# Optimization experiments

Measured on AMD Instinct MI355X. Metric: run time of the kernel, lower is better.

Reference implementation:

```python
import jax, jax.numpy as jnp
import numpy as np

N_NODES = 50000
N_EDGES = 800000
NUM_GRAPHS = 512


def gcn_conv(x, edge_index, W, b, num_nodes):
    # PyG GCNConv: h = D^{-1/2} (A + I) D^{-1/2} (x @ W) + b
    h = x @ W
    src, dst = edge_index[0], edge_index[1]
    loop = jnp.arange(num_nodes)
    src = jnp.concatenate([src, loop])
    dst = jnp.concatenate([dst, loop])
    deg = jax.ops.segment_sum(jnp.ones_like(dst, dtype=h.dtype), dst,
                              num_segments=num_nodes)
    dinv = jnp.where(deg > 0, jax.lax.rsqrt(deg), 0.0)
    norm = dinv[src] * dinv[dst]                      # [E+N]
    msg = h[src] * norm[:, None]                      # gather + scale
    out = jax.ops.segment_sum(msg, dst, num_segments=num_nodes)  # scatter-add
    return out + b


def global_mean_pool(x, batch, num_graphs):
    sums = jax.ops.segment_sum(x, batch, num_segments=num_graphs)
    cnts = jax.ops.segment_sum(jnp.ones((x.shape[0],), x.dtype), batch,
                               num_segments=num_graphs)
    return sums / jnp.maximum(cnts, 1.0)[:, None]


def setup_inputs() -> dict:
    key = jax.random.key(0)
    ks = jax.random.split(key, 8)
    x = jax.random.normal(ks[0], (N_NODES, 128), dtype=jnp.float32)
    edge_index = jax.random.randint(ks[1], (2, N_EDGES), 0, N_NODES, dtype=jnp.int64)
    batch = jnp.sort(jax.random.randint(ks[2], (N_NODES,), 0, NUM_GRAPHS, dtype=jnp.int64))
    W1 = jax.random.normal(ks[3], (128, 128), dtype=jnp.float32) * (1.0 / np.sqrt(128))
    b1 = jnp.zeros((128,), jnp.float32)
    W2 = jax.random.normal(ks[4], (128, 64), dtype=jnp.float32) * (1.0 / np.sqrt(128))
    b2 = jnp.zeros((64,), jnp.float32)
    Wl = jax.random.normal(ks[5], (64, 64), dtype=jnp.float32) * (1.0 / np.sqrt(64))
    bl = jnp.zeros((64,), jnp.float32)
    return {"x": x, "edge_index": edge_index, "batch": batch,
            "W1": W1, "b1": b1, "W2": W2, "b2": b2, "Wl": Wl, "bl": bl}


def reference(x, edge_index, batch, W1, b1, W2, b2, Wl, bl):
    num_nodes = x.shape[0]
    h = gcn_conv(x, edge_index, W1, b1, num_nodes)
    h = jax.nn.relu(h)
    h = gcn_conv(h, edge_index, W2, b2, num_nodes)
    g = global_mean_pool(h, batch, NUM_GRAPHS)
    # dropout p=0.5 is identity in eval mode
    return g @ Wl + bl
```

## Files before the change

### kernel.cpp

```cpp
#include <hip/hip_runtime.h>
#include <hip/hip_fp16.h>
#include <math.h>


#define FEAT1 128
#define FEAT2 64
#define BCAP 8192

using half8 = __attribute__((ext_vector_type(8))) _Float16;
using half4 = __attribute__((ext_vector_type(4))) _Float16;
using f32x4 = __attribute__((ext_vector_type(4))) float;


__global__ __launch_bounds__(256) void bin_scatter(const int* __restrict__ esrc,
                                                   const int* __restrict__ edst,
                                                   int ne, int nb,
                                                   int* __restrict__ bucket_cursor,
                                                   int* __restrict__ ebin) {
    __shared__ int lcnt[256];
    __shared__ int lcur[256];
    const int tid = threadIdx.x;
    const int e0 = blockIdx.x * 8192;
    lcnt[tid] = 0;
    __syncthreads();
    #pragma unroll 4
    for (int k = 0; k < 32; k++) {
        int e = e0 + k * 256 + tid;
        if (e < ne) atomicAdd(&lcnt[edst[e] >> 8], 1);
    }
    __syncthreads();
    if (tid < nb && lcnt[tid] > 0)
        lcur[tid] = atomicAdd(&bucket_cursor[tid], lcnt[tid]);
    __syncthreads();
    #pragma unroll 4
    for (int k = 0; k < 32; k++) {
        int e = e0 + k * 256 + tid;
        if (e < ne) {
            int d = edst[e];
            int b = d >> 8;
            int p = atomicAdd(&lcur[b], 1);
            if (p < BCAP)
                ebin[b * BCAP + p] = esrc[e] | ((d & 255) << 18);
        }
    }
}

__global__ __launch_bounds__(256) void bucket_csr(const int* __restrict__ ebin,
                                                  const int* __restrict__ bucket_cursor,
                                                  int n_nodes,
                                                  int* __restrict__ csr,
                                                  int2* __restrict__ nodeinfo,
                                                  float* __restrict__ dinv) {
    __shared__ int lcnt[256];
    __shared__ int lscan[256];
    __shared__ int lcur[256];
    const int b = blockIdx.x;
    const int tid = threadIdx.x;
    const int ebeg = b * BCAP;
    int cnt_b = bucket_cursor[b];
    if (cnt_b > BCAP) cnt_b = BCAP;
    const int eend = ebeg + cnt_b;
    lcnt[tid] = 0;
    __syncthreads();
    for (int e = ebeg + tid; e < eend; e += 256)
        atomicAdd(&lcnt[(ebin[e] >> 18) & 255], 1);
    __syncthreads();
    int v = lcnt[tid];
    lscan[tid] = v;
    __syncthreads();
    for (int off = 1; off < 256; off <<= 1) {
        int u = (tid >= off) ? lscan[tid - off] : 0;
        __syncthreads();
        lscan[tid] += u;
        __syncthreads();
    }
    const int start = ebeg + (lscan[tid] - v);
    const int node = (b << 8) + tid;
    if (node < n_nodes) {
        nodeinfo[node] = make_int2(start, v);
        dinv[node] = (float)(1.0 / sqrt((double)(v + 1)));
    }
    lcur[tid] = start;
    __syncthreads();
    for (int e = ebeg + tid; e < eend; e += 256) {
        int pk = ebin[e];
        int p = atomicAdd(&lcur[(pk >> 18) & 255], 1);
        csr[p] = pk & 0x3FFFF;
    }
}

template <int FOUT, bool A_F16>
__global__ __launch_bounds__(256) void gemm_mfma(const void* __restrict__ Aptr,
                                                 const float* __restrict__ W,
                                                 const float* __restrict__ dinv,
                                                 _Float16* __restrict__ out, int n) {
    __shared__ _Float16 As[128 * 136];
    __shared__ _Float16 Ws[64 * 136];
    const int tid = threadIdx.x;
    const int wv = tid >> 6;
    const int lane = tid & 63;
    constexpr int NCT = FOUT / 64;
    const int row0 = blockIdx.x * 128;

    {
        const int r = tid >> 1;
        const int c0 = (tid & 1) * 64;
        const int grow = row0 + r;
        if constexpr (A_F16) {
            const _Float16* A = (const _Float16*)Aptr + (size_t)grow * 128 + c0;
            #pragma unroll
            for (int j = 0; j < 8; j++) {
                half8 v = {};
                if (grow < n) v = *(const half8*)(A + j * 8);
                *(half8*)(&As[r * 136 + c0 + j * 8]) = v;
            }
        } else {
            const float* A = (const float*)Aptr + (size_t)grow * 128 + c0;
            #pragma unroll
            for (int j = 0; j < 16; j++) {
                float4 v = {0.f, 0.f, 0.f, 0.f};
                if (grow < n) v = *(const float4*)(A + j * 4);
                half4 hv = {(_Float16)v.x, (_Float16)v.y, (_Float16)v.z, (_Float16)v.w};
                *(half4*)(&As[r * 136 + c0 + j * 4]) = hv;
            }
        }
    }

    for (int ct = 0; ct < NCT; ct++) {
        const int col0 = ct * 64;
        __syncthreads();
        {
            const int k = tid >> 1;
            const int cb = (tid & 1) * 32;
            #pragma unroll
            for (int j = 0; j < 8; j++) {
                int c = cb + j * 4;
                float4 v = *(const float4*)(W + (size_t)k * FOUT + col0 + c);
                Ws[(c + 0) * 136 + k] = (_Float16)v.x;
                Ws[(c + 1) * 136 + k] = (_Float16)v.y;
                Ws[(c + 2) * 136 + k] = (_Float16)v.z;
                Ws[(c + 3) * 136 + k] = (_Float16)v.w;
            }
        }
        __syncthreads();

        f32x4 acc[2][4] = {};
        const int mrow = wv * 32 + (lane & 15);
        const int kb = (lane >> 4) * 8;
        #pragma unroll
        for (int ks = 0; ks < 4; ks++) {
            const int kk = ks * 32 + kb;
            half8 a0 = *(const half8*)(&As[mrow * 136 + kk]);
            half8 a1 = *(const half8*)(&As[(mrow + 16) * 136 + kk]);
            #pragma unroll
            for (int nj = 0; nj < 4; nj++) {
                half8 b = *(const half8*)(&Ws[(nj * 16 + (lane & 15)) * 136 + kk]);
                acc[0][nj] = __builtin_amdgcn_mfma_f32_16x16x32_f16(a0, b, acc[0][nj], 0, 0, 0);
                acc[1][nj] = __builtin_amdgcn_mfma_f32_16x16x32_f16(a1, b, acc[1][nj], 0, 0, 0);
            }
        }

        #pragma unroll
        for (int mi = 0; mi < 2; mi++) {
            const int gr0 = row0 + wv * 32 + mi * 16 + (lane >> 4) * 4;
            #pragma unroll
            for (int r = 0; r < 4; r++) {
                const int grow = gr0 + r;
                if (grow < n) {
                    const float s = dinv[grow];
                    #pragma unroll
                    for (int nj = 0; nj < 4; nj++) {
                        out[(size_t)grow * FOUT + col0 + nj * 16 + (lane & 15)] =
                            (_Float16)(acc[mi][nj][r] * s);
                    }
                }
            }
        }
    }
}

template <int F, bool RELU, bool OUT16>
__global__ __launch_bounds__(256) void aggregate_h(const __half* __restrict__ t,
                                                   const float* __restrict__ dinv,
                                                   const int2* __restrict__ nodeinfo,
                                                   const int* __restrict__ csr_src,
                                                   const float* __restrict__ bias,
                                                   void* __restrict__ outp, int n) {
    const int wv = threadIdx.x >> 6;
    const int lane = threadIdx.x & 63;
    const int i = blockIdx.x * 4 + wv;
    if (i >= n) return;
    const float di = dinv[i];
    const int2 ni = nodeinfo[i];
    const int e0 = ni.x, e1 = ni.x + ni.y;

    if constexpr (F == 128) {
        float2 a0, a1 = {0.f, 0.f}, a2 = {0.f, 0.f}, a3 = {0.f, 0.f};
        a0 = __half22float2(((const __half2*)(t + (size_t)i * F))[lane]);
        int e = e0;
        for (; e + 8 <= e1; e += 8) {
            int s0 = csr_src[e + 0], s1 = csr_src[e + 1], s2 = csr_src[e + 2], s3 = csr_src[e + 3];
            int s4 = csr_src[e + 4], s5 = csr_src[e + 5], s6 = csr_src[e + 6], s7 = csr_src[e + 7];
            float2 v0 = __half22float2(((const __half2*)(t + (size_t)s0 * F))[lane]);
            float2 v1 = __half22float2(((const __half2*)(t + (size_t)s1 * F))[lane]);
            float2 v2 = __half22float2(((const __half2*)(t + (size_t)s2 * F))[lane]);
            float2 v3 = __half22float2(((const __half2*)(t + (size_t)s3 * F))[lane]);
            float2 v4 = __half22float2(((const __half2*)(t + (size_t)s4 * F))[lane]);
            float2 v5 = __half22float2(((const __half2*)(t + (size_t)s5 * F))[lane]);
            float2 v6 = __half22float2(((const __half2*)(t + (size_t)s6 * F))[lane]);
            float2 v7 = __half22float2(((const __half2*)(t + (size_t)s7 * F))[lane]);
            a0.x += v0.x + v4.x; a0.y += v0.y + v4.y;
            a1.x += v1.x + v5.x; a1.y += v1.y + v5.y;
            a2.x += v2.x + v6.x; a2.y += v2.y + v6.y;
            a3.x += v3.x + v7.x; a3.y += v3.y + v7.y;
        }
        for (; e + 4 <= e1; e += 4) {
            int s0 = csr_src[e + 0], s1 = csr_src[e + 1], s2 = csr_src[e + 2], s3 = csr_src[e + 3];
            float2 v0 = __half22float2(((const __half2*)(t + (size_t)s0 * F))[lane]);
            float2 v1 = __half22float2(((const __half2*)(t + (size_t)s1 * F))[lane]);
            float2 v2 = __half22float2(((const __half2*)(t + (size_t)s2 * F))[lane]);
            float2 v3 = __half22float2(((const __half2*)(t + (size_t)s3 * F))[lane]);
            a0.x += v0.x; a0.y += v0.y;
            a1.x += v1.x; a1.y += v1.y;
            a2.x += v2.x; a2.y += v2.y;
            a3.x += v3.x; a3.y += v3.y;
        }
        for (; e < e1; e++) {
            int s = csr_src[e];
            float2 v = __half22float2(((const __half2*)(t + (size_t)s * F))[lane]);
            a0.x += v.x; a0.y += v.y;
        }
        float2 b = ((const float2*)bias)[lane];
        float rx = (a0.x + a1.x + a2.x + a3.x) * di + b.x;
        float ry = (a0.y + a1.y + a2.y + a3.y) * di + b.y;
        if (RELU) { rx = fmaxf(rx, 0.f); ry = fmaxf(ry, 0.f); }
        if constexpr (OUT16) {
            ((__half2*)((__half*)outp + (size_t)i * F))[lane] = __floats2half2_rn(rx, ry);
        } else {
            ((float2*)((float*)outp + (size_t)i * F))[lane] = make_float2(rx, ry);
        }
    } else {
        float a0, a1 = 0.f, a2 = 0.f, a3 = 0.f;
        a0 = __half2float(t[(size_t)i * F + lane]);
        int e = e0;
        for (; e + 8 <= e1; e += 8) {
            int s0 = csr_src[e + 0], s1 = csr_src[e + 1], s2 = csr_src[e + 2], s3 = csr_src[e + 3];
            int s4 = csr_src[e + 4], s5 = csr_src[e + 5], s6 = csr_src[e + 6], s7 = csr_src[e + 7];
            float v0 = __half2float(t[(size_t)s0 * F + lane]);
            float v1 = __half2float(t[(size_t)s1 * F + lane]);
            float v2 = __half2float(t[(size_t)s2 * F + lane]);
            float v3 = __half2float(t[(size_t)s3 * F + lane]);
            float v4 = __half2float(t[(size_t)s4 * F + lane]);
            float v5 = __half2float(t[(size_t)s5 * F + lane]);
            float v6 = __half2float(t[(size_t)s6 * F + lane]);
            float v7 = __half2float(t[(size_t)s7 * F + lane]);
            a0 += v0 + v4; a1 += v1 + v5; a2 += v2 + v6; a3 += v3 + v7;
        }
        for (; e + 4 <= e1; e += 4) {
            int s0 = csr_src[e + 0], s1 = csr_src[e + 1], s2 = csr_src[e + 2], s3 = csr_src[e + 3];
            a0 += __half2float(t[(size_t)s0 * F + lane]);
            a1 += __half2float(t[(size_t)s1 * F + lane]);
            a2 += __half2float(t[(size_t)s2 * F + lane]);
            a3 += __half2float(t[(size_t)s3 * F + lane]);
        }
        for (; e < e1; e++) {
            a0 += __half2float(t[(size_t)csr_src[e] * F + lane]);
        }
        float r = (a0 + a1 + a2 + a3) * di + bias[lane];
        if (RELU) r = fmaxf(r, 0.f);
        if constexpr (OUT16) {
            ((__half*)outp)[(size_t)i * F + lane] = __float2half(r);
        } else {
            ((float*)outp)[(size_t)i * F + lane] = r;
        }
    }
}

__global__ __launch_bounds__(256) void pool_classify(const float* __restrict__ h2,
                                                     const int* __restrict__ batch, int n,
                                                     const float* __restrict__ Wl,
                                                     const float* __restrict__ bl,
                                                     float* __restrict__ out) {
    __shared__ float partial[4][64];
    __shared__ float pooled_s[64];
    const int g = blockIdx.x;
    const int wv = threadIdx.x >> 6;
    const int lane = threadIdx.x & 63;

    int lo = 0, hi = n;
    while (lo < hi) { int mid = (lo + hi) >> 1; if (batch[mid] < g) lo = mid + 1; else hi = mid; }
    const int start = lo;
    hi = n;
    while (lo < hi) { int mid = (lo + hi) >> 1; if (batch[mid] < g + 1) lo = mid + 1; else hi = mid; }
    const int end = lo;

    float sum = 0.0f;
    int r = start + wv;
    for (; r + 8 <= end; r += 8) {
        float v0 = h2[(size_t)r * 64 + lane];
        float v1 = h2[(size_t)(r + 4) * 64 + lane];
        sum += v0 + v1;
    }
    for (; r < end; r += 4) sum += h2[(size_t)r * 64 + lane];
    partial[wv][lane] = sum;
    __syncthreads();

    if (wv == 0) {
        float s = partial[0][lane] + partial[1][lane] + partial[2][lane] + partial[3][lane];
        float cnt = (float)(end - start);
        pooled_s[lane] = s / fmaxf(cnt, 1.0f);
    }
    __syncthreads();

    if (wv == 0) {
        float acc = bl[lane];
        #pragma unroll 8
        for (int k = 0; k < 64; k++) acc += pooled_s[k] * Wl[k * 64 + lane];
        out[(size_t)g * 64 + lane] = acc;
    }
}


extern "C" void kernel_launch(void* const* d_in, const int* in_sizes, int n_in,
                              void* d_out, int out_size, void* d_ws, size_t ws_size,
                              hipStream_t stream) {
    const float* x    = (const float*)d_in[0];
    const int*   eidx = (const int*)d_in[1];
    const int*   batch= (const int*)d_in[2];
    const float* W1   = (const float*)d_in[3];
    const float* b1   = (const float*)d_in[4];
    const float* W2   = (const float*)d_in[5];
    const float* b2   = (const float*)d_in[6];
    const float* Wl   = (const float*)d_in[7];
    const float* bl   = (const float*)d_in[8];
    float* out = (float*)d_out;

    const int n_nodes  = in_sizes[0] / FEAT1;
    const int n_edges  = in_sizes[1] / 2;
    const int n_graphs = out_size / FEAT2;
    const int* esrc = eidx;
    const int* edst = eidx + n_edges;
    const int nb = (n_nodes + 255) >> 8;

    char* ws = (char*)d_ws;
    size_t off = 0;
    auto alloc = [&](size_t bytes) -> void* {
        void* p = ws + off;
        off += (bytes + 255) & ~(size_t)255;
        return p;
    };
    _Float16* t1     = (_Float16*)alloc((size_t)n_nodes * FEAT1 * 2);
    __half*   h1h    = (__half*)alloc((size_t)n_nodes * FEAT1 * 2);
    float*    h2     = (float*)alloc((size_t)n_nodes * FEAT2 * 4);
    float*    dinv   = (float*)alloc((size_t)n_nodes * 4);
    int2*   nodeinfo = (int2*)alloc((size_t)n_nodes * 8);
    int*    bcur     = (int*)alloc((size_t)nb * 4);
    int*    ebin     = (int*)alloc((size_t)nb * BCAP * 4);
    int*    csr      = (int*)alloc((size_t)nb * BCAP * 4);

    const int nrb = (n_nodes + 127) / 128;

    hipMemsetAsync(bcur, 0, (size_t)nb * 4, stream);
    bin_scatter<<<(n_edges + 8191) / 8192, 256, 0, stream>>>(esrc, edst, n_edges, nb, bcur, ebin);
    bucket_csr<<<nb, 256, 0, stream>>>(ebin, bcur, n_nodes, csr, nodeinfo, dinv);

    gemm_mfma<FEAT1, false><<<nrb, 256, 0, stream>>>(x, W1, dinv, t1, n_nodes);
    aggregate_h<FEAT1, true, true><<<(n_nodes + 3) / 4, 256, 0, stream>>>(
        (const __half*)t1, dinv, nodeinfo, csr, b1, h1h, n_nodes);

    gemm_mfma<FEAT2, true><<<nrb, 256, 0, stream>>>(h1h, W2, dinv, t1, n_nodes);
    aggregate_h<FEAT2, false, false><<<(n_nodes + 3) / 4, 256, 0, stream>>>(
        (const __half*)t1, dinv, nodeinfo, csr, b2, h2, n_nodes);

    pool_classify<<<n_graphs, 256, 0, stream>>>(h2, batch, n_nodes, Wl, bl, out);
}
```

Before: 152.9 us.

## Fuse layer-2 aggregation with mean-pool via atomics and cache edge dst in bin_scatter

After: 151.8 us. About the same (-0.7%).

```diff
diff --git a/kernel.cpp b/kernel.cpp
--- a/kernel.cpp
+++ b/kernel.cpp
@@ -21,22 +21,24 @@
     __shared__ int lcur[256];
     const int tid = threadIdx.x;
     const int e0 = blockIdx.x * 8192;
+    int dcache[32];
     lcnt[tid] = 0;
     __syncthreads();
-    #pragma unroll 4
+    #pragma unroll
     for (int k = 0; k < 32; k++) {
         int e = e0 + k * 256 + tid;
-        if (e < ne) atomicAdd(&lcnt[edst[e] >> 8], 1);
+        dcache[k] = (e < ne) ? edst[e] : -1;
+        if (dcache[k] >= 0) atomicAdd(&lcnt[dcache[k] >> 8], 1);
     }
     __syncthreads();
     if (tid < nb && lcnt[tid] > 0)
         lcur[tid] = atomicAdd(&bucket_cursor[tid], lcnt[tid]);
     __syncthreads();
-    #pragma unroll 4
+    #pragma unroll
     for (int k = 0; k < 32; k++) {
-        int e = e0 + k * 256 + tid;
-        if (e < ne) {
-            int d = edst[e];
+        int d = dcache[k];
+        if (d >= 0) {
+            int e = e0 + k * 256 + tid;
             int b = d >> 8;
             int p = atomicAdd(&lcur[b], 1);
             if (p < BCAP)
@@ -179,13 +181,13 @@
     }
 }
 
-template <int F, bool RELU, bool OUT16>
-__global__ __launch_bounds__(256) void aggregate_h(const __half* __restrict__ t,
-                                                   const float* __restrict__ dinv,
-                                                   const int2* __restrict__ nodeinfo,
-                                                   const int* __restrict__ csr_src,
-                                                   const float* __restrict__ bias,
-                                                   void* __restrict__ outp, int n) {
+__global__ __launch_bounds__(256) void aggregate_l1(const __half* __restrict__ t,
+                                                    const float* __restrict__ dinv,
+                                                    const int2* __restrict__ nodeinfo,
+                                                    const int* __restrict__ csr_src,
+                                                    const float* __restrict__ bias,
+                                                    __half* __restrict__ outp, int n) {
+    constexpr int F = 128;
     const int wv = threadIdx.x >> 6;
     const int lane = threadIdx.x & 63;
     const int i = blockIdx.x * 4 + wv;
@@ -194,130 +196,116 @@
     const int2 ni = nodeinfo[i];
     const int e0 = ni.x, e1 = ni.x + ni.y;
 
-    if constexpr (F == 128) {
-        float2 a0, a1 = {0.f, 0.f}, a2 = {0.f, 0.f}, a3 = {0.f, 0.f};
-        a0 = __half22float2(((const __half2*)(t + (size_t)i * F))[lane]);
-        int e = e0;
-        for (; e + 8 <= e1; e += 8) {
-            int s0 = csr_src[e + 0], s1 = csr_src[e + 1], s2 = csr_src[e + 2], s3 = csr_src[e + 3];
-            int s4 = csr_src[e + 4], s5 = csr_src[e + 5], s6 = csr_src[e + 6], s7 = csr_src[e + 7];
-            float2 v0 = __half22float2(((const __half2*)(t + (size_t)s0 * F))[lane]);
-            float2 v1 = __half22float2(((const __half2*)(t + (size_t)s1 * F))[lane]);
-            float2 v2 = __half22float2(((const __half2*)(t + (size_t)s2 * F))[lane]);
-            float2 v3 = __half22float2(((const __half2*)(t + (size_t)s3 * F))[lane]);
-            float2 v4 = __half22float2(((const __half2*)(t + (size_t)s4 * F))[lane]);
-            float2 v5 = __half22float2(((const __half2*)(t + (size_t)s5 * F))[lane]);
-            float2 v6 = __half22float2(((const __half2*)(t + (size_t)s6 * F))[lane]);
-            float2 v7 = __half22float2(((const __half2*)(t + (size_t)s7 * F))[lane]);
-            a0.x += v0.x + v4.x; a0.y += v0.y + v4.y;
-            a1.x += v1.x + v5.x; a1.y += v1.y + v5.y;
-            a2.x += v2.x + v6.x; a2.y += v2.y + v6.y;
-            a3.x += v3.x + v7.x; a3.y += v3.y + v7.y;
-        }
-        for (; e + 4 <= e1; e += 4) {
-            int s0 = csr_src[e + 0], s1 = csr_src[e + 1], s2 = csr_src[e + 2], s3 = csr_src[e + 3];
-            float2 v0 = __half22float2(((const __half2*)(t + (size_t)s0 * F))[lane]);
-            float2 v1 = __half22float2(((const __half2*)(t + (size_t)s1 * F))[lane]);
-            float2 v2 = __half22float2(((const __half2*)(t + (size_t)s2 * F))[lane]);
-            float2 v3 = __half22float2(((const __half2*)(t + (size_t)s3 * F))[lane]);
-            a0.x += v0.x; a0.y += v0.y;
-            a1.x += v1.x; a1.y += v1.y;
-            a2.x += v2.x; a2.y += v2.y;
-            a3.x += v3.x; a3.y += v3.y;
-        }
-        for (; e < e1; e++) {
-            int s = csr_src[e];
-            float2 v = __half22float2(((const __half2*)(t + (size_t)s * F))[lane]);
-            a0.x += v.x; a0.y += v.y;
-        }
-        float2 b = ((const float2*)bias)[lane];
-        float rx = (a0.x + a1.x + a2.x + a3.x) * di + b.x;
-        float ry = (a0.y + a1.y + a2.y + a3.y) * di + b.y;
-        if (RELU) { rx = fmaxf(rx, 0.f); ry = fmaxf(ry, 0.f); }
-        if constexpr (OUT16) {
-            ((__half2*)((__half*)outp + (size_t)i * F))[lane] = __floats2half2_rn(rx, ry);
-        } else {
-            ((float2*)((float*)outp + (size_t)i * F))[lane] = make_float2(rx, ry);
-        }
-    } else {
-        float a0, a1 = 0.f, a2 = 0.f, a3 = 0.f;
-        a0 = __half2float(t[(size_t)i * F + lane]);
-        int e = e0;
-        for (; e + 8 <= e1; e += 8) {
-            int s0 = csr_src[e + 0], s1 = csr_src[e + 1], s2 = csr_src[e + 2], s3 = csr_src[e + 3];
-            int s4 = csr_src[e + 4], s5 = csr_src[e + 5], s6 = csr_src[e + 6], s7 = csr_src[e + 7];
-            float v0 = __half2float(t[(size_t)s0 * F + lane]);
-            float v1 = __half2float(t[(size_t)s1 * F + lane]);
-            float v2 = __half2float(t[(size_t)s2 * F + lane]);
-            float v3 = __half2float(t[(size_t)s3 * F + lane]);
-            float v4 = __half2float(t[(size_t)s4 * F + lane]);
-            float v5 = __half2float(t[(size_t)s5 * F + lane]);
-            float v6 = __half2float(t[(size_t)s6 * F + lane]);
-            float v7 = __half2float(t[(size_t)s7 * F + lane]);
-            a0 += v0 + v4; a1 += v1 + v5; a2 += v2 + v6; a3 += v3 + v7;
-        }
-        for (; e + 4 <= e1; e += 4) {
-            int s0 = csr_src[e + 0], s1 = csr_src[e + 1], s2 = csr_src[e + 2], s3 = csr_src[e + 3];
-            a0 += __half2float(t[(size_t)s0 * F + lane]);
-            a1 += __half2float(t[(size_t)s1 * F + lane]);
-            a2 += __half2float(t[(size_t)s2 * F + lane]);
-            a3 += __half2float(t[(size_t)s3 * F + lane]);
-        }
-        for (; e < e1; e++) {
-            a0 += __half2float(t[(size_t)csr_src[e] * F + lane]);
-        }
-        float r = (a0 + a1 + a2 + a3) * di + bias[lane];
-        if (RELU) r = fmaxf(r, 0.f);
-        if constexpr (OUT16) {
-            ((__half*)outp)[(size_t)i * F + lane] = __float2half(r);
-        } else {
-            ((float*)outp)[(size_t)i * F + lane] = r;
-        }
-    }
-}
-
-__global__ __launch_bounds__(256) void pool_classify(const float* __restrict__ h2,
-                                                     const int* __restrict__ batch, int n,
-                                                     const float* __restrict__ Wl,
-                                                     const float* __restrict__ bl,
-                                                     float* __restrict__ out) {
-    __shared__ float partial[4][64];
-    __shared__ float pooled_s[64];
-    const int g = blockIdx.x;
+    float2 a0, a1 = {0.f, 0.f}, a2 = {0.f, 0.f}, a3 = {0.f, 0.f};
+    a0 = __half22float2(((const __half2*)(t + (size_t)i * F))[lane]);
+    int e = e0;
+    for (; e + 8 <= e1; e += 8) {
+        int s0 = csr_src[e + 0], s1 = csr_src[e + 1], s2 = csr_src[e + 2], s3 = csr_src[e + 3];
+        int s4 = csr_src[e + 4], s5 = csr_src[e + 5], s6 = csr_src[e + 6], s7 = csr_src[e + 7];
+        float2 v0 = __half22float2(((const __half2*)(t + (size_t)s0 * F))[lane]);
+        float2 v1 = __half22float2(((const __half2*)(t + (size_t)s1 * F))[lane]);
+        float2 v2 = __half22float2(((const __half2*)(t + (size_t)s2 * F))[lane]);
+        float2 v3 = __half22float2(((const __half2*)(t + (size_t)s3 * F))[lane]);
+        float2 v4 = __half22float2(((const __half2*)(t + (size_t)s4 * F))[lane]);
+        float2 v5 = __half22float2(((const __half2*)(t + (size_t)s5 * F))[lane]);
+        float2 v6 = __half22float2(((const __half2*)(t + (size_t)s6 * F))[lane]);
+        float2 v7 = __half22float2(((const __half2*)(t + (size_t)s7 * F))[lane]);
+        a0.x += v0.x + v4.x; a0.y += v0.y + v4.y;
+        a1.x += v1.x + v5.x; a1.y += v1.y + v5.y;
+        a2.x += v2.x + v6.x; a2.y += v2.y + v6.y;
+        a3.x += v3.x + v7.x; a3.y += v3.y + v7.y;
+    }
+    for (; e + 4 <= e1; e += 4) {
+        int s0 = csr_src[e + 0], s1 = csr_src[e + 1], s2 = csr_src[e + 2], s3 = csr_src[e + 3];
+        float2 v0 = __half22float2(((const __half2*)(t + (size_t)s0 * F))[lane]);
+        float2 v1 = __half22float2(((const __half2*)(t + (size_t)s1 * F))[lane]);
+        float2 v2 = __half22float2(((const __half2*)(t + (size_t)s2 * F))[lane]);
+        float2 v3 = __half22float2(((const __half2*)(t + (size_t)s3 * F))[lane]);
+        a0.x += v0.x; a0.y += v0.y;
+        a1.x += v1.x; a1.y += v1.y;
+        a2.x += v2.x; a2.y += v2.y;
+        a3.x += v3.x; a3.y += v3.y;
+    }
+    for (; e < e1; e++) {
+        int s = csr_src[e];
+        float2 v = __half22float2(((const __half2*)(t + (size_t)s * F))[lane]);
+        a0.x += v.x; a0.y += v.y;
+    }
+    float2 b = ((const float2*)bias)[lane];
+    float rx = (a0.x + a1.x + a2.x + a3.x) * di + b.x;
+    float ry = (a0.y + a1.y + a2.y + a3.y) * di + b.y;
+    rx = fmaxf(rx, 0.f); ry = fmaxf(ry, 0.f);
+    ((__half2*)(outp + (size_t)i * F))[lane] = __floats2half2_rn(rx, ry);
+}
+
+__global__ __launch_bounds__(256) void aggregate_pool(const __half* __restrict__ t,
+                                                      const float* __restrict__ dinv,
+                                                      const int2* __restrict__ nodeinfo,
+                                                      const int* __restrict__ csr_src,
+                                                      const int* __restrict__ batch,
+                                                      float* __restrict__ pooled_sums, int n) {
+    constexpr int F = 64;
     const int wv = threadIdx.x >> 6;
     const int lane = threadIdx.x & 63;
-
+    const int i = blockIdx.x * 4 + wv;
+    if (i >= n) return;
+    const float di = dinv[i];
+    const int2 ni = nodeinfo[i];
+    const int e0 = ni.x, e1 = ni.x + ni.y;
+
+    float a0, a1 = 0.f, a2 = 0.f, a3 = 0.f;
+    a0 = __half2float(t[(size_t)i * F + lane]);
+    int e = e0;
+    for (; e + 8 <= e1; e += 8) {
+        int s0 = csr_src[e + 0], s1 = csr_src[e + 1], s2 = csr_src[e + 2], s3 = csr_src[e + 3];
+        int s4 = csr_src[e + 4], s5 = csr_src[e + 5], s6 = csr_src[e + 6], s7 = csr_src[e + 7];
+        float v0 = __half2float(t[(size_t)s0 * F + lane]);
+        float v1 = __half2float(t[(size_t)s1 * F + lane]);
+        float v2 = __half2float(t[(size_t)s2 * F + lane]);
+        float v3 = __half2float(t[(size_t)s3 * F + lane]);
+        float v4 = __half2float(t[(size_t)s4 * F + lane]);
+        float v5 = __half2float(t[(size_t)s5 * F + lane]);
+        float v6 = __half2float(t[(size_t)s6 * F + lane]);
+        float v7 = __half2float(t[(size_t)s7 * F + lane]);
+        a0 += v0 + v4; a1 += v1 + v5; a2 += v2 + v6; a3 += v3 + v7;
+    }
+    for (; e + 4 <= e1; e += 4) {
+        int s0 = csr_src[e + 0], s1 = csr_src[e + 1], s2 = csr_src[e + 2], s3 = csr_src[e + 3];
+        a0 += __half2float(t[(size_t)s0 * F + lane]);
+        a1 += __half2float(t[(size_t)s1 * F + lane]);
+        a2 += __half2float(t[(size_t)s2 * F + lane]);
+        a3 += __half2float(t[(size_t)s3 * F + lane]);
+    }
+    for (; e < e1; e++) {
+        a0 += __half2float(t[(size_t)csr_src[e] * F + lane]);
+    }
+    float r = (a0 + a1 + a2 + a3) * di;
+    const int g = batch[i];
+    atomicAdd(&pooled_sums[(size_t)g * F + lane], r);
+}
+
+__global__ __launch_bounds__(64) void classify(const float* __restrict__ pooled_sums,
+                                               const int* __restrict__ batch, int n,
+                                               const float* __restrict__ b2,
+                                               const float* __restrict__ Wl,
+                                               const float* __restrict__ bl,
+                                               float* __restrict__ out) {
+    __shared__ float pr[64];
+    const int g = blockIdx.x;
+    const int lane = threadIdx.x;
     int lo = 0, hi = n;
     while (lo < hi) { int mid = (lo + hi) >> 1; if (batch[mid] < g) lo = mid + 1; else hi = mid; }
     const int start = lo;
     hi = n;
     while (lo < hi) { int mid = (lo + hi) >> 1; if (batch[mid] < g + 1) lo = mid + 1; else hi = mid; }
-    const int end = lo;
-
-    float sum = 0.0f;
-    int r = start + wv;
-    for (; r + 8 <= end; r += 8) {
-        float v0 = h2[(size_t)r * 64 + lane];
-        float v1 = h2[(size_t)(r + 4) * 64 + lane];
-        sum += v0 + v1;
-    }
-    for (; r < end; r += 4) sum += h2[(size_t)r * 64 + lane];
-    partial[wv][lane] = sum;
-    __syncthreads();
-
-    if (wv == 0) {
-        float s = partial[0][lane] + partial[1][lane] + partial[2][lane] + partial[3][lane];
-        float cnt = (float)(end - start);
-        pooled_s[lane] = s / fmaxf(cnt, 1.0f);
-    }
-    __syncthreads();
-
-    if (wv == 0) {
-        float acc = bl[lane];
-        #pragma unroll 8
-        for (int k = 0; k < 64; k++) acc += pooled_s[k] * Wl[k * 64 + lane];
-        out[(size_t)g * 64 + lane] = acc;
-    }
+    const float cnt = (float)(lo - start);
+    float p = pooled_sums[(size_t)g * 64 + lane] / fmaxf(cnt, 1.0f) + b2[lane];
+    pr[lane] = p;
+    __syncthreads();
+    float acc = bl[lane];
+    #pragma unroll 8
+    for (int k = 0; k < 64; k++) acc += pr[k] * Wl[k * 64 + lane];
+    out[(size_t)g * 64 + lane] = acc;
 }
 
 
@@ -351,26 +339,27 @@
     };
     _Float16* t1     = (_Float16*)alloc((size_t)n_nodes * FEAT1 * 2);
     __half*   h1h    = (__half*)alloc((size_t)n_nodes * FEAT1 * 2);
-    float*    h2     = (float*)alloc((size_t)n_nodes * FEAT2 * 4);
     float*    dinv   = (float*)alloc((size_t)n_nodes * 4);
     int2*   nodeinfo = (int2*)alloc((size_t)n_nodes * 8);
     int*    bcur     = (int*)alloc((size_t)nb * 4);
+    float*  pooled   = (float*)alloc((size_t)n_graphs * FEAT2 * 4);
+    char*   zend     = (char*)alloc(0);
     int*    ebin     = (int*)alloc((size_t)nb * BCAP * 4);
     int*    csr      = (int*)alloc((size_t)nb * BCAP * 4);
 
     const int nrb = (n_nodes + 127) / 128;
 
-    hipMemsetAsync(bcur, 0, (size_t)nb * 4, stream);
+    hipMemsetAsync(bcur, 0, (size_t)(zend - (char*)bcur), stream);
     bin_scatter<<<(n_edges + 8191) / 8192, 256, 0, stream>>>(esrc, edst, n_edges, nb, bcur, ebin);
     bucket_csr<<<nb, 256, 0, stream>>>(ebin, bcur, n_nodes, csr, nodeinfo, dinv);
 
     gemm_mfma<FEAT1, false><<<nrb, 256, 0, stream>>>(x, W1, dinv, t1, n_nodes);
-    aggregate_h<FEAT1, true, true><<<(n_nodes + 3) / 4, 256, 0, stream>>>(
+    aggregate_l1<<<(n_nodes + 3) / 4, 256, 0, stream>>>(
         (const __half*)t1, dinv, nodeinfo, csr, b1, h1h, n_nodes);
 
     gemm_mfma<FEAT2, true><<<nrb, 256, 0, stream>>>(h1h, W2, dinv, t1, n_nodes);
-    aggregate_h<FEAT2, false, false><<<(n_nodes + 3) / 4, 256, 0, stream>>>(
-        (const __half*)t1, dinv, nodeinfo, csr, b2, h2, n_nodes);
-
-    pool_classify<<<n_graphs, 256, 0, stream>>>(h2, batch, n_nodes, Wl, bl, out);
-}
+    aggregate_pool<<<(n_nodes + 3) / 4, 256, 0, stream>>>(
+        (const __half*)t1, dinv, nodeinfo, csr, batch, pooled, n_nodes);
+
+    classify<<<n_graphs, 64, 0, stream>>>(pooled, batch, n_nodes, b2, Wl, bl, out);
+}
```
